# Optimization experiments

Hardware: AMD Instinct MI355X
Metric: run time of the kernel (lower is better)

The kernel has to match this reference:

```python
import jax, jax.numpy as jnp
import numpy as np

T, B, D_IN, D_LAT, D_OUT = 2048, 64, 256, 256, 256


def _linear_params(key, fan_in, fan_out):
    kw, kb = jax.random.split(key)
    bound = 1.0 / np.sqrt(fan_in)
    W = jax.random.uniform(kw, (fan_out, fan_in), jnp.float32, -bound, bound)
    b = jax.random.uniform(kb, (fan_out,), jnp.float32, -bound, bound)
    return W, b


def setup_inputs() -> dict:
    key = jax.random.key(0)
    ks = jax.random.split(key, 6)
    Wf, bf = _linear_params(ks[0], D_IN + D_LAT, D_LAT)
    Wi, bi = _linear_params(ks[1], D_IN + D_LAT, D_LAT)
    Wo, bo = _linear_params(ks[2], D_IN + D_LAT, D_LAT)
    Wc, bc = _linear_params(ks[3], D_IN + D_LAT, D_LAT)
    Wout, bout = _linear_params(ks[4], D_LAT, D_OUT)
    x = jax.random.normal(ks[5], (T, B, D_IN), jnp.float32)
    h0 = jnp.zeros((B, D_LAT), jnp.float32)
    C0 = jnp.zeros((B, D_LAT), jnp.float32)
    return {"x": x, "h0": h0, "C0": C0,
            "Wf": Wf, "bf": bf, "Wi": Wi, "bi": bi,
            "Wo": Wo, "bo": bo, "Wc": Wc, "bc": bc,
            "Wout": Wout, "bout": bout}


def reference(x, h0, C0, Wf, bf, Wi, bi, Wo, bo, Wc, bc, Wout, bout):
    def step(carry, x_t):
        h, C = carry
        comb = jnp.concatenate([x_t, h], axis=-1)  # [B, D_IN+D_LAT]
        f_t = jax.nn.sigmoid(comb @ Wf.T + bf)
        i_t = jax.nn.sigmoid(comb @ Wi.T + bi)
        o_t = jax.nn.sigmoid(comb @ Wo.T + bo)
        C_tilde = jnp.tanh(comb @ Wc.T + bc)
        C_new = f_t * C + i_t * C_tilde
        h_new = o_t * jnp.tanh(C_new)
        out = h_new @ Wout.T + bout
        return (h_new, C_new), (out, h_new)
    (h_f, C_f), (outputs, hidden_states) = jax.lax.scan(step, (h0, C0), x)
    return outputs, hidden_states, C_f
```

## Files before the change

### kernel.cpp

```cpp
#include <hip/hip_runtime.h>
#include <cstdint>
#include <cstddef>

#define T_STEPS 2048
#define BATCH 64

typedef _Float16 f16;
typedef _Float16 f16x2 __attribute__((ext_vector_type(2)));
typedef _Float16 f16x8 __attribute__((ext_vector_type(8)));
typedef float f32x4 __attribute__((ext_vector_type(4)));
typedef unsigned int uint32;
typedef unsigned long long uint64;
typedef uint32 u32x4 __attribute__((ext_vector_type(4)));

__device__ __forceinline__ float dot2(uint32 w, uint32 h, float c) {
  f16x2 a = __builtin_bit_cast(f16x2, w);
  f16x2 b = __builtin_bit_cast(f16x2, h);
  return __builtin_amdgcn_fdot2(a, b, c, false);
}

__device__ __forceinline__ float dot8(u32x4 w, u32x4 h, float c) {
  c = dot2(w[0], h[0], c);
  c = dot2(w[1], h[1], c);
  c = dot2(w[2], h[2], c);
  c = dot2(w[3], h[3], c);
  return c;
}

__device__ __forceinline__ uint32 pack2(f16 a, f16 b) {
  f16x2 t; t[0] = a; t[1] = b;
  return __builtin_bit_cast(uint32, t);
}

__global__ __launch_bounds__(256) void setup_weights(
    const float* __restrict__ Wf, const float* __restrict__ Wi,
    const float* __restrict__ Wo, const float* __restrict__ Wc,
    const float* __restrict__ Wout,
    f16* __restrict__ wx16, f16* __restrict__ wout16, uint32* __restrict__ whp)
{
  int id = blockIdx.x * 256 + threadIdx.x;
  const float* WG_[4] = {Wf, Wi, Wo, Wc};
  if (id < 262144) {
    int n = id >> 8, k = id & 255;
    int G = n >> 8, j = n & 255;
    wx16[id] = (f16)WG_[G][j * 512 + k];
    return;
  }
  id -= 262144;
  if (id < 65536) { wout16[id] = (f16)Wout[id]; return; }
  id -= 65536;
  if (id < 131072) {
    int kq = id >> 12, rem = id & 4095;
    int o = rem >> 2, c = rem & 3;
    int G = o >> 8, j = o & 255;
    const float* src = WG_[G] + j * 512 + 256 + kq * 8 + c * 2;
    whp[id] = pack2((f16)src[0], (f16)src[1]);
  }
}

__global__ __launch_bounds__(256) void setup_state(
    const float* __restrict__ h0, const float* __restrict__ C0,
    uint64* __restrict__ hbuf, float* __restrict__ c32)
{
  int id = blockIdx.x * 256 + threadIdx.x;
  if (id < 8192) {
    int slot = id >> 5, i = id & 31;
    int r = slot >> 2, q = slot & 3;
    const float* hr = h0 + r * 256 + q * 64 + 2 * i;
    uint32 a = (uint32)__builtin_bit_cast(unsigned short, (f16)hr[0]);
    uint32 b = (uint32)__builtin_bit_cast(unsigned short, (f16)hr[1]);
    hbuf[id] = ((uint64)b << 32) | (uint64)a;
    return;
  }
  id -= 8192;
  if (id < 8192) { hbuf[8192 + id] = 0xFFFF0000FFFF0000ULL; return; }
  id -= 8192;
  if (id < 16384) c32[id] = C0[id];
}

template<int A_F32, int OUT_F32_BIAS>
__global__ __launch_bounds__(256) void gemm_k(
    const void* __restrict__ Av, const f16* __restrict__ B,
    void* __restrict__ Cv, const float* __restrict__ bias, int N)
{
  constexpr int LDA = 264;
  __shared__ f16 As[128 * 264];
  __shared__ f16 Bs[128 * 264];
  const int tid = threadIdx.x;
  const int m0 = blockIdx.x * 128;
  const int n0 = blockIdx.y * 128;

  if (A_F32) {
    const float* A = (const float*)Av;
    #pragma unroll
    for (int j = 0; j < 32; ++j) {
      int flat = (tid + j * 256) * 4;
      int row = flat >> 8, col = flat & 255;
      const float4 v = *(const float4*)(A + (size_t)(m0 + row) * 256 + col);
      uint2 u; u.x = pack2((f16)v.x, (f16)v.y); u.y = pack2((f16)v.z, (f16)v.w);
      *(uint2*)&As[row * LDA + col] = u;
    }
  } else {
    const f16* A = (const f16*)Av;
    #pragma unroll
    for (int j = 0; j < 32; ++j) {
      int flat = (tid + j * 256) * 4;
      int row = flat >> 8, col = flat & 255;
      *(uint2*)&As[row * LDA + col] = *(const uint2*)(A + (size_t)(m0 + row) * 256 + col);
    }
  }
  #pragma unroll
  for (int j = 0; j < 32; ++j) {
    int flat = (tid + j * 256) * 4;
    int row = flat >> 8, col = flat & 255;
    *(uint2*)&Bs[row * LDA + col] = *(const uint2*)(B + (size_t)(n0 + row) * 256 + col);
  }
  __syncthreads();

  const int wave = tid >> 6, l = tid & 63;
  const int wr = wave >> 1, wc = wave & 1;
  const int lr = l & 15, lq = l >> 4;

  f32x4 acc[4][4] = {};
  #pragma unroll
  for (int kk = 0; kk < 8; ++kk) {
    f16x8 a[4], b[4];
    #pragma unroll
    for (int mi = 0; mi < 4; ++mi)
      a[mi] = *(const f16x8*)&As[(64 * wr + 16 * mi + lr) * LDA + kk * 32 + lq * 8];
    #pragma unroll
    for (int ni = 0; ni < 4; ++ni)
      b[ni] = *(const f16x8*)&Bs[(64 * wc + 16 * ni + lr) * LDA + kk * 32 + lq * 8];
    #pragma unroll
    for (int mi = 0; mi < 4; ++mi)
      #pragma unroll
      for (int ni = 0; ni < 4; ++ni)
        acc[mi][ni] = __builtin_amdgcn_mfma_f32_16x16x32_f16(a[mi], b[ni], acc[mi][ni], 0, 0, 0);
  }

  #pragma unroll
  for (int mi = 0; mi < 4; ++mi) {
    #pragma unroll
    for (int ni = 0; ni < 4; ++ni) {
      int col = n0 + 64 * wc + 16 * ni + lr;
      float bv = 0.f;
      if (OUT_F32_BIAS) bv = bias[col];
      #pragma unroll
      for (int v = 0; v < 4; ++v) {
        int row = m0 + 64 * wr + 16 * mi + lq * 4 + v;
        if (OUT_F32_BIAS) ((float*)Cv)[(size_t)row * N + col] = acc[mi][ni][v] + bv;
        else              ((f16*)Cv)[(size_t)row * N + col] = (f16)acc[mi][ni][v];
      }
    }
  }
}

#define RL20(M) M(0) M(1) M(2) M(3) M(4) M(5) M(6) M(7) M(8) M(9) M(10) M(11) \
  M(12) M(13) M(14) M(15) M(16) M(17) M(18) M(19)

__global__ __launch_bounds__(256) void lstm_persist(
    const uint32* __restrict__ whp,
    const float* __restrict__ bf, const float* __restrict__ bi,
    const float* __restrict__ bo, const float* __restrict__ bc,
    const f16* __restrict__ xproj, uint64* __restrict__ hbuf,
    float* __restrict__ c32, float* __restrict__ hid_out,
    f16* __restrict__ h16c, float* __restrict__ cf_out, int t0, int Tc)
{
  __shared__ u32x4 wlds[12 * 256];
  __shared__ uint32 h_lds[128] __attribute__((aligned(16)));
  __shared__ float part[4 * 68];
  __shared__ unsigned short hstage[64];

  const int tid = threadIdx.x;
  const int w = blockIdx.x;
  const int q = w >> 6, r = w & 63;
  const int G = tid >> 6, col = tid & 63;
  const int j = q * 64 + col;
  const int o = (G << 8) + j;

  const u32x4* wq = (const u32x4*)whp;

#define LOADW(i) u32x4 w##i = wq[(i) * 1024 + o];
  RL20(LOADW)
#undef LOADW
  #pragma unroll
  for (int i = 0; i < 12; ++i)
    wlds[i * 256 + tid] = wq[(20 + i) * 1024 + o];

  const float* bGp = (G == 0) ? bf : (G == 1) ? bi : (G == 2) ? bo : bc;
  const float biasv = bGp[j];

  float Creg = 0.f;
  if (tid < 64) Creg = c32[r * 256 + q * 64 + tid];

  uint64* mybuf = hbuf + (size_t)(r * 4 + q) * 32;

  for (int tl = 0; tl < Tc; ++tl) {
    const int gt = t0 + tl;
    const int pp = gt & 1;

    const float xpv = (float)xproj[((size_t)tl * 64 + r) * 1024 + o];

    if (tid < 96) {
      const int s = tid >> 5, i = tid & 31;
      const int qq = s + (s >= q ? 1 : 0);
      const uint64* p = hbuf + (size_t)pp * 8192 + (size_t)(r * 4 + qq) * 32 + i;
      const uint32 tg = (uint32)gt;
      uint64 v = __hip_atomic_load(p, __ATOMIC_RELAXED, __HIP_MEMORY_SCOPE_AGENT);
      int tries = 0;
      while (((((uint32)v) >> 16) != tg || ((uint32)(v >> 48)) != tg) &&
             ++tries < (1 << 20)) {
        v = __hip_atomic_load(p, __ATOMIC_RELAXED, __HIP_MEMORY_SCOPE_AGENT);
      }
      h_lds[qq * 32 + i] =
          (((uint32)v) & 0xFFFFu) | ((((uint32)(v >> 32)) & 0xFFFFu) << 16);
    } else if (tl == 0 && tid < 128) {
      const int i = tid - 96;
      const uint64* p = mybuf + (size_t)pp * 8192 + i;
      const uint32 tg = (uint32)gt;
      uint64 v = __hip_atomic_load(p, __ATOMIC_RELAXED, __HIP_MEMORY_SCOPE_AGENT);
      int tries = 0;
      while (((((uint32)v) >> 16) != tg || ((uint32)(v >> 48)) != tg) &&
             ++tries < (1 << 20)) {
        v = __hip_atomic_load(p, __ATOMIC_RELAXED, __HIP_MEMORY_SCOPE_AGENT);
      }
      h_lds[q * 32 + i] =
          (((uint32)v) & 0xFFFFu) | ((((uint32)(v >> 32)) & 0xFFFFu) << 16);
    }
    __syncthreads();

    int otid;
    asm volatile("v_mov_b32 %0, %1" : "=v"(otid) : "v"(tid));
    float ac[4] = {0.f, 0.f, 0.f, 0.f};
#define DOTW(i) { const u32x4 hh = *(const u32x4*)&h_lds[(i) * 4]; \
                  ac[(i) & 3] = dot8(w##i, hh, ac[(i) & 3]); }
    RL20(DOTW)
#undef DOTW
    #pragma unroll
    for (int i = 0; i < 12; ++i) {
      const u32x4 hh = *(const u32x4*)&h_lds[(20 + i) * 4];
      ac[(20 + i) & 3] = dot8(wlds[i * 256 + otid], hh, ac[(20 + i) & 3]);
    }
    part[G * 68 + col] = (ac[0] + ac[1]) + (ac[2] + ac[3]) + xpv + biasv;
    __syncthreads();

    if (tid < 64) {
      const float pf = part[tid];
      const float pi = part[68 + tid];
      const float po = part[136 + tid];
      const float pc = part[204 + tid];
      const float f_ = __builtin_amdgcn_rcpf(1.f + __expf(-pf));
      const float i_ = __builtin_amdgcn_rcpf(1.f + __expf(-pi));
      const float o_ = __builtin_amdgcn_rcpf(1.f + __expf(-po));
      const float cb = 1.f - 2.f * __builtin_amdgcn_rcpf(__expf(2.f * pc) + 1.f);
      const float Cn = f_ * Creg + i_ * cb;
      Creg = Cn;
      const float th = 1.f - 2.f * __builtin_amdgcn_rcpf(__expf(2.f * Cn) + 1.f);
      const float hn = o_ * th;
      const int jg = q * 64 + tid;
      hid_out[((size_t)gt * 64 + r) * 256 + jg] = hn;
      const f16 h16v = (f16)hn;
      hstage[tid] = __builtin_bit_cast(unsigned short, h16v);
      h16c[((size_t)tl * 64 + r) * 256 + jg] = h16v;
      if (gt == T_STEPS - 1) cf_out[r * 256 + jg] = Cn;
    }
    __syncthreads();

    if (tid < 32) {
      const uint32 a = (uint32)hstage[2 * tid];
      const uint32 b = (uint32)hstage[2 * tid + 1];
      h_lds[q * 32 + tid] = a | (b << 16);
      const uint32 tg1u = ((uint32)(gt + 1)) << 16;
      const uint64 v = ((uint64)(b | tg1u) << 32) | (uint64)(a | tg1u);
      __hip_atomic_store(mybuf + (size_t)((gt + 1) & 1) * 8192 + tid, v,
                         __ATOMIC_RELAXED, __HIP_MEMORY_SCOPE_AGENT);
    }
  }

  if (tid < 64) c32[r * 256 + q * 64 + tid] = Creg;
}

extern "C" void kernel_launch(void* const* d_in, const int* in_sizes, int n_in,
                              void* d_out, int out_size, void* d_ws, size_t ws_size,
                              hipStream_t stream)
{
  const float* x    = (const float*)d_in[0];
  const float* h0   = (const float*)d_in[1];
  const float* C0   = (const float*)d_in[2];
  const float* Wf   = (const float*)d_in[3];
  const float* bf   = (const float*)d_in[4];
  const float* Wi   = (const float*)d_in[5];
  const float* bi   = (const float*)d_in[6];
  const float* Wo   = (const float*)d_in[7];
  const float* bo   = (const float*)d_in[8];
  const float* Wc   = (const float*)d_in[9];
  const float* bc   = (const float*)d_in[10];
  const float* Wout = (const float*)d_in[11];
  const float* bout = (const float*)d_in[12];
  float* out = (float*)d_out;

  char* w = (char*)d_ws;
  f16*    wx16   = (f16*)w;    w += (size_t)1024 * 256 * 2;
  f16*    wout16 = (f16*)w;    w += (size_t)256 * 256 * 2;
  uint32* whp    = (uint32*)w; w += (size_t)131072 * 4;
  uint64* hbuf   = (uint64*)w; w += (size_t)2 * 8192 * 8;
  float*  c32    = (float*)w;  w += (size_t)64 * 256 * 4;
  const size_t fixedB = (size_t)(w - (char*)d_ws);

  int Tc = 2;
  const int cands[] = {2048, 1024, 512, 256, 128, 64, 32, 16, 8, 4, 2};
  for (int c : cands) {
    if (fixedB + (size_t)c * 163840 <= ws_size) { Tc = c; break; }
  }

  f16* xproj = (f16*)w;
  f16* h16c  = (f16*)(w + (size_t)Tc * 64 * 1024 * 2);

  setup_weights<<<1792, 256, 0, stream>>>(Wf, Wi, Wo, Wc, Wout,
                                          wx16, wout16, whp);
  setup_state<<<128, 256, 0, stream>>>(h0, C0, hbuf, c32);

  float* hid_out = out + (size_t)T_STEPS * 64 * 256;
  float* cf_out  = out + (size_t)2 * T_STEPS * 64 * 256;

  for (int t0 = 0; t0 < T_STEPS; t0 += Tc) {
    gemm_k<1, 0><<<dim3(Tc * 64 / 128, 8), 256, 0, stream>>>(
        x + (size_t)t0 * 64 * 256, wx16, xproj, nullptr, 1024);
    lstm_persist<<<256, 256, 0, stream>>>(whp, bf, bi, bo, bc,
                                          xproj, hbuf, c32,
                                          hid_out, h16c, cf_out, t0, Tc);
    gemm_k<0, 1><<<dim3(Tc * 64 / 128, 2), 256, 0, stream>>>(
        h16c, wout16, out + (size_t)t0 * 64 * 256, bout, 256);
  }
}
```

Baseline: 3.813 ms.

## Split LSTM recurrence across 512 blocks with K-halved register-resident weights

The persistent recurrent kernel now uses 8 blocks per batch row, each owning 32 hidden units, instead of 4 blocks owning 64. Each pair of threads splits the 256-wide K dimension, holding all weights in registers, which removes the LDS weight spill. The pair combines partial sums with a shuffle, and the h publish step packs values with shuffles, dropping one __syncthreads per step. In exchange there are twice as many blocks to synchronise through the global flag buffer, with 7 remote slices polled per step, and occupancy of 512 blocks on the device must hold for the spin-wait scheme to avoid deadlock.

```diff
diff --git a/kernel.cpp b/kernel.cpp
--- a/kernel.cpp
+++ b/kernel.cpp
@@ -64,9 +64,9 @@
 {
   int id = blockIdx.x * 256 + threadIdx.x;
   if (id < 8192) {
-    int slot = id >> 5, i = id & 31;
-    int r = slot >> 2, q = slot & 3;
-    const float* hr = h0 + r * 256 + q * 64 + 2 * i;
+    int slot = id >> 4, i = id & 15;
+    int r = slot >> 3, e = slot & 7;
+    const float* hr = h0 + r * 256 + 32 * e + 2 * i;
     uint32 a = (uint32)__builtin_bit_cast(unsigned short, (f16)hr[0]);
     uint32 b = (uint32)__builtin_bit_cast(unsigned short, (f16)hr[1]);
     hbuf[id] = ((uint64)b << 32) | (uint64)a;
@@ -155,8 +155,8 @@
   }
 }
 
-#define RL20(M) M(0) M(1) M(2) M(3) M(4) M(5) M(6) M(7) M(8) M(9) M(10) M(11) \
-  M(12) M(13) M(14) M(15) M(16) M(17) M(18) M(19)
+#define RL16(M) M(0) M(1) M(2) M(3) M(4) M(5) M(6) M(7) M(8) M(9) M(10) M(11) \
+  M(12) M(13) M(14) M(15)
 
 __global__ __launch_bounds__(256) void lstm_persist(
     const uint32* __restrict__ whp,
@@ -166,89 +166,85 @@
     float* __restrict__ c32, float* __restrict__ hid_out,
     f16* __restrict__ h16c, float* __restrict__ cf_out, int t0, int Tc)
 {
-  __shared__ u32x4 wlds[12 * 256];
   __shared__ uint32 h_lds[128] __attribute__((aligned(16)));
-  __shared__ float part[4 * 68];
-  __shared__ unsigned short hstage[64];
+  __shared__ float part[132];
 
   const int tid = threadIdx.x;
   const int w = blockIdx.x;
-  const int q = w >> 6, r = w & 63;
-  const int G = tid >> 6, col = tid & 63;
-  const int j = q * 64 + col;
-  const int o = (G << 8) + j;
+  const int e = w & 7;
+  const int r = w >> 3;
+  const int o_local = tid >> 1;
+  const int kh = tid & 1;
+  const int g = o_local >> 5, c = o_local & 31;
+  const int jglob = 32 * e + c;
+  const int o_glob = (g << 8) + jglob;
 
   const u32x4* wq = (const u32x4*)whp;
 
-#define LOADW(i) u32x4 w##i = wq[(i) * 1024 + o];
-  RL20(LOADW)
+#define LOADW(i) u32x4 wr##i = wq[(16 * kh + (i)) * 1024 + o_glob];
+  RL16(LOADW)
 #undef LOADW
-  #pragma unroll
-  for (int i = 0; i < 12; ++i)
-    wlds[i * 256 + tid] = wq[(20 + i) * 1024 + o];
-
-  const float* bGp = (G == 0) ? bf : (G == 1) ? bi : (G == 2) ? bo : bc;
-  const float biasv = bGp[j];
+
+  const float* bGp = (g == 0) ? bf : (g == 1) ? bi : (g == 2) ? bo : bc;
+  const float biasv = bGp[jglob];
 
   float Creg = 0.f;
-  if (tid < 64) Creg = c32[r * 256 + q * 64 + tid];
-
-  uint64* mybuf = hbuf + (size_t)(r * 4 + q) * 32;
+  if (tid < 32) Creg = c32[r * 256 + 32 * e + tid];
+
+  uint64* mybuf = hbuf + (size_t)(r * 8 + e) * 16;
 
   for (int tl = 0; tl < Tc; ++tl) {
     const int gt = t0 + tl;
     const int pp = gt & 1;
 
-    const float xpv = (float)xproj[((size_t)tl * 64 + r) * 1024 + o];
-
-    if (tid < 96) {
-      const int s = tid >> 5, i = tid & 31;
-      const int qq = s + (s >= q ? 1 : 0);
-      const uint64* p = hbuf + (size_t)pp * 8192 + (size_t)(r * 4 + qq) * 32 + i;
+    float xpv = 0.f;
+    if (!kh) xpv = (float)xproj[((size_t)tl * 64 + r) * 1024 + o_glob];
+
+    if (tid < 112) {
+      const int s = tid >> 4, i = tid & 15;
+      const int ee = s + (s >= e ? 1 : 0);
+      const uint64* p = hbuf + (size_t)pp * 8192 + (size_t)(r * 8 + ee) * 16 + i;
       const uint32 tg = (uint32)gt;
       uint64 v = __hip_atomic_load(p, __ATOMIC_RELAXED, __HIP_MEMORY_SCOPE_AGENT);
       int tries = 0;
       while (((((uint32)v) >> 16) != tg || ((uint32)(v >> 48)) != tg) &&
-             ++tries < (1 << 20)) {
+             ++tries < (1 << 22)) {
         v = __hip_atomic_load(p, __ATOMIC_RELAXED, __HIP_MEMORY_SCOPE_AGENT);
       }
-      h_lds[qq * 32 + i] =
+      h_lds[16 * ee + i] =
           (((uint32)v) & 0xFFFFu) | ((((uint32)(v >> 32)) & 0xFFFFu) << 16);
     } else if (tl == 0 && tid < 128) {
-      const int i = tid - 96;
+      const int i = tid - 112;
       const uint64* p = mybuf + (size_t)pp * 8192 + i;
       const uint32 tg = (uint32)gt;
       uint64 v = __hip_atomic_load(p, __ATOMIC_RELAXED, __HIP_MEMORY_SCOPE_AGENT);
       int tries = 0;
       while (((((uint32)v) >> 16) != tg || ((uint32)(v >> 48)) != tg) &&
-             ++tries < (1 << 20)) {
+             ++tries < (1 << 22)) {
         v = __hip_atomic_load(p, __ATOMIC_RELAXED, __HIP_MEMORY_SCOPE_AGENT);
       }
-      h_lds[q * 32 + i] =
+      h_lds[16 * e + i] =
           (((uint32)v) & 0xFFFFu) | ((((uint32)(v >> 32)) & 0xFFFFu) << 16);
     }
     __syncthreads();
 
-    int otid;
-    asm volatile("v_mov_b32 %0, %1" : "=v"(otid) : "v"(tid));
-    float ac[4] = {0.f, 0.f, 0.f, 0.f};
-#define DOTW(i) { const u32x4 hh = *(const u32x4*)&h_lds[(i) * 4]; \
-                  ac[(i) & 3] = dot8(w##i, hh, ac[(i) & 3]); }
-    RL20(DOTW)
+    float a0 = 0.f, a1 = 0.f, a2 = 0.f, a3 = 0.f;
+#define DOTW(i) { const u32x4 hh = *(const u32x4*)&h_lds[(16 * kh + (i)) * 4]; \
+                  float& A_ = (((i) & 3) == 0) ? a0 : (((i) & 3) == 1) ? a1 \
+                            : (((i) & 3) == 2) ? a2 : a3; \
+                  A_ = dot8(wr##i, hh, A_); }
+    RL16(DOTW)
 #undef DOTW
-    #pragma unroll
-    for (int i = 0; i < 12; ++i) {
-      const u32x4 hh = *(const u32x4*)&h_lds[(20 + i) * 4];
-      ac[(20 + i) & 3] = dot8(wlds[i * 256 + otid], hh, ac[(20 + i) & 3]);
-    }
-    part[G * 68 + col] = (ac[0] + ac[1]) + (ac[2] + ac[3]) + xpv + biasv;
+    float acc = (a0 + a1) + (a2 + a3);
+    acc += __shfl_xor(acc, 1, 64);
+    if (!kh) part[o_local] = acc + xpv + biasv;
     __syncthreads();
 
-    if (tid < 64) {
+    if (tid < 32) {
       const float pf = part[tid];
-      const float pi = part[68 + tid];
-      const float po = part[136 + tid];
-      const float pc = part[204 + tid];
+      const float pi = part[32 + tid];
+      const float po = part[64 + tid];
+      const float pc = part[96 + tid];
       const float f_ = __builtin_amdgcn_rcpf(1.f + __expf(-pf));
       const float i_ = __builtin_amdgcn_rcpf(1.f + __expf(-pi));
       const float o_ = __builtin_amdgcn_rcpf(1.f + __expf(-po));
@@ -257,27 +253,26 @@
       Creg = Cn;
       const float th = 1.f - 2.f * __builtin_amdgcn_rcpf(__expf(2.f * Cn) + 1.f);
       const float hn = o_ * th;
-      const int jg = q * 64 + tid;
+      const int jg = 32 * e + tid;
       hid_out[((size_t)gt * 64 + r) * 256 + jg] = hn;
       const f16 h16v = (f16)hn;
-      hstage[tid] = __builtin_bit_cast(unsigned short, h16v);
       h16c[((size_t)tl * 64 + r) * 256 + jg] = h16v;
       if (gt == T_STEPS - 1) cf_out[r * 256 + jg] = Cn;
-    }
-    __syncthreads();
-
-    if (tid < 32) {
-      const uint32 a = (uint32)hstage[2 * tid];
-      const uint32 b = (uint32)hstage[2 * tid + 1];
-      h_lds[q * 32 + tid] = a | (b << 16);
-      const uint32 tg1u = ((uint32)(gt + 1)) << 16;
-      const uint64 v = ((uint64)(b | tg1u) << 32) | (uint64)(a | tg1u);
-      __hip_atomic_store(mybuf + (size_t)((gt + 1) & 1) * 8192 + tid, v,
-                         __ATOMIC_RELAXED, __HIP_MEMORY_SCOPE_AGENT);
-    }
-  }
-
-  if (tid < 64) c32[r * 256 + q * 64 + tid] = Creg;
+
+      const uint32 hb = (uint32)__builtin_bit_cast(unsigned short, h16v);
+      const uint32 lo = (uint32)__shfl((int)hb, 2 * tid, 64);
+      const uint32 hi = (uint32)__shfl((int)hb, 2 * tid + 1, 64);
+      if (tid < 16) {
+        h_lds[16 * e + tid] = lo | (hi << 16);
+        const uint32 tg1u = ((uint32)(gt + 1)) << 16;
+        const uint64 v = ((uint64)(hi | tg1u) << 32) | (uint64)(lo | tg1u);
+        __hip_atomic_store(mybuf + (size_t)((gt + 1) & 1) * 8192 + tid, v,
+                           __ATOMIC_RELAXED, __HIP_MEMORY_SCOPE_AGENT);
+      }
+    }
+  }
+
+  if (tid < 32) c32[r * 256 + 32 * e + tid] = Creg;
 }
 
 extern "C" void kernel_launch(void* const* d_in, const int* in_sizes, int n_in,
@@ -326,7 +321,7 @@
   for (int t0 = 0; t0 < T_STEPS; t0 += Tc) {
     gemm_k<1, 0><<<dim3(Tc * 64 / 128, 8), 256, 0, stream>>>(
         x + (size_t)t0 * 64 * 256, wx16, xproj, nullptr, 1024);
-    lstm_persist<<<256, 256, 0, stream>>>(whp, bf, bi, bo, bc,
+    lstm_persist<<<512, 256, 0, stream>>>(whp, bf, bi, bo, bc,
                                           xproj, hbuf, c32,
                                           hid_out, h16c, cf_out, t0, Tc);
     gemm_k<0, 1><<<dim3(Tc * 64 / 128, 2), 256, 0, stream>>>(
```

Result: faster. 3.615 ms (-5.2%).
